# Kernel tuning notes

Hardware: AMD Instinct MI355X
Metric: run time of the kernel (lower is better)

## Reference

```python
import jax, jax.numpy as jnp
import numpy as np

B, T, E = 8, 1024, 512
H = 1024            # hidden_dim
NH, QD, VD = 4, 256, 512
C1, C2 = 512, 2     # conv1_out, conv2_out
K, PAD = 3, 1


def conv1d(x, w, b, pad):
    # x: [B, Cin, T], w: [Cout, Cin, K]
    y = jax.lax.conv_general_dilated(x, w, (1,), [(pad, pad)],
                                     dimension_numbers=('NCH', 'OIH', 'NCH'))
    return y + b[None, :, None]


def setup_inputs() -> dict:
    key = jax.random.key(0)
    ks = jax.random.split(key, 24)
    n = lambda i, shape, s=0.02: jax.random.normal(ks[i], shape, dtype=jnp.float32) * s
    inp = {
        'x':    jax.random.normal(ks[0], (B, T, E), dtype=jnp.float32),
        # in_pro: two 1x1 convs over channels (acting as linears)
        'w_in1': n(1, (E, E)), 'b_in1': jnp.zeros((E,), jnp.float32),
        'w_in2': n(2, (E, E)), 'b_in2': jnp.zeros((E,), jnp.float32),
        # attention projections
        'w_q': n(3, (NH * QD, E), float(np.sqrt(2.0 / (E + QD)))), 'b_q': jnp.zeros((NH * QD,), jnp.float32),
        'w_k': n(4, (NH * QD, E), float(np.sqrt(2.0 / (E + QD)))), 'b_k': jnp.zeros((NH * QD,), jnp.float32),
        'w_v': n(5, (NH * VD, E), float(np.sqrt(2.0 / (E + VD)))), 'b_v': jnp.zeros((NH * VD,), jnp.float32),
        # output projection (1x1 conv)
        'w_p': n(6, (E, NH * VD)), 'b_p': jnp.zeros((E,), jnp.float32),
        # layernorm
        'ln_g': jnp.ones((E,), jnp.float32), 'ln_b': jnp.zeros((E,), jnp.float32),
        # LSTM (1 layer, unidirectional, hidden H)
        'w_ih': n(7, (4 * H, E)), 'w_hh': n(8, (4 * H, H)),
        'b_ih': jnp.zeros((4 * H,), jnp.float32), 'b_hh': jnp.zeros((4 * H,), jnp.float32),
        # attention pooling convs
        'w_c1': n(9, (C1, H, K)), 'b_c1': jnp.zeros((C1,), jnp.float32),
        'w_c2': n(10, (C2, C1, K)), 'b_c2': jnp.zeros((C2,), jnp.float32),
    }
    return inp


def reference(x, w_in1, b_in1, w_in2, b_in2, w_q, b_q, w_k, b_k, w_v, b_v,
              w_p, b_p, ln_g, ln_b, w_ih, w_hh, b_ih, b_hh,
              w_c1, b_c1, w_c2, b_c2):
    # in_pro: 1x1 conv -> LeakyReLU(0.25) -> 1x1 conv (channel-wise linears)
    h = jnp.einsum('bte,fe->btf', x, w_in1) + b_in1
    h = jnp.where(h >= 0, h, 0.25 * h)
    h = jnp.einsum('bte,fe->btf', h, w_in2) + b_in2  # [B,T,E]

    # multi-head attention (no scale factor, as in the source)
    q = (jnp.einsum('bte,fe->btf', h, w_q) + b_q).reshape(B, T, NH, QD)
    k = (jnp.einsum('bte,fe->btf', h, w_k) + b_k).reshape(B, T, NH, QD)
    v = (jnp.einsum('bte,fe->btf', h, w_v) + b_v).reshape(B, T, NH, VD)
    scores = jnp.einsum('btnd,bsnd->bnts', q, k)          # [B,NH,T,T]
    attn = jax.nn.softmax(scores, axis=-1)
    o = jnp.einsum('bnts,bsnd->btnd', attn, v)            # [B,T,NH,VD]
    o = o.reshape(B, T, NH * VD)

    # p_conv1 (1x1) then LayerNorm over E
    y = jnp.einsum('btc,ec->bte', o, w_p) + b_p           # [B,T,E]
    mu = jnp.mean(y, axis=-1, keepdims=True)
    var = jnp.mean(jnp.square(y - mu), axis=-1, keepdims=True)
    y = (y - mu) * jax.lax.rsqrt(var + 1e-5) * ln_g + ln_b

    # LSTM (batch_first, 1 layer); dropout is identity in eval mode
    def step(carry, xt):
        hprev, cprev = carry
        g = xt @ w_ih.T + hprev @ w_hh.T + b_ih + b_hh    # [B,4H]
        i, f, gg, og = jnp.split(g, 4, axis=-1)
        c = jax.nn.sigmoid(f) * cprev + jax.nn.sigmoid(i) * jnp.tanh(gg)
        hn = jax.nn.sigmoid(og) * jnp.tanh(c)
        return (hn, c), hn
    init = (jnp.zeros((B, H), y.dtype), jnp.zeros((B, H), y.dtype))
    _, hs = jax.lax.scan(step, init, jnp.swapaxes(y, 0, 1))  # [T,B,H]
    lstm_out = jnp.swapaxes(hs, 0, 1)                        # [B,T,H]

    # conv-based attention pooling
    a = conv1d(jnp.swapaxes(lstm_out, 1, 2), w_c1, b_c1, PAD)  # [B,C1,T]
    a = jax.nn.relu(a)
    a = conv1d(a, w_c2, b_c2, PAD)                              # [B,C2,T]
    a = jax.nn.softmax(a, axis=2)
    feat = jnp.einsum('bct,bth->bch', a, lstm_out)              # [B,C2,H]
    return feat.reshape(B, C2 * H)
```

## Files before the change

### kernel.cpp

```cpp
#include <hip/hip_runtime.h>
#include <stdint.h>

typedef short short8 __attribute__((ext_vector_type(8)));
typedef float float4v __attribute__((ext_vector_type(4)));

__device__ __forceinline__ float b2f(short s) {
    return __uint_as_float(((unsigned)(unsigned short)s) << 16);
}
__device__ __forceinline__ short f2b(float f) {
    unsigned u = __float_as_uint(f);
    unsigned r = (u + 0x7fffu + ((u >> 16) & 1u)) >> 16;
    return (short)r;
}

__global__ void k_f32_to_bf16(const float* __restrict__ in, short* __restrict__ out, int n) {
    int i = blockIdx.x * blockDim.x + threadIdx.x;
    int stride = gridDim.x * blockDim.x;
    for (; i < n; i += stride) out[i] = f2b(in[i]);
}

__global__ void k_wc1_tr(const float* __restrict__ in, short* __restrict__ out) {
    int i = blockIdx.x * blockDim.x + threadIdx.x;
    if (i >= 512 * 3072) return;
    int c = i / 3072, rr = i % 3072, dk = rr / 1024, h = rr % 1024;
    out[i] = f2b(in[(c * 1024 + h) * 3 + dk]);
}

__global__ void k_bias_sum(const float* __restrict__ a, const float* __restrict__ b,
                           float* __restrict__ o, int n) {
    int i = blockIdx.x * blockDim.x + threadIdx.x;
    if (i < n) o[i] = a[i] + b[i];
}

__global__ __launch_bounds__(256) void k_gemm_bt(
    const short* __restrict__ A, const short* __restrict__ B,
    float* __restrict__ Cf, short* __restrict__ Cb,
    const float* __restrict__ bias,
    int M, int N, int K, int lda, int ldb, int ldc,
    int z0n, long sA0, long sA1, long sB0, long sB1, long sC0, long sC1,
    int act, int gap)
{
    __shared__ __align__(16) short lds[2 * 128 * 32];
    const int z = blockIdx.z;
    const int z0 = z % z0n, z1 = z / z0n;
    A += z1 * sA1 + z0 * sA0;
    B += z1 * sB1 + z0 * sB0;
    const long coff = z1 * sC1 + z0 * sC0;
    const int tn0 = blockIdx.x * 128, tm0 = blockIdx.y * 128;
    const int tid = threadIdx.x, ln = tid & 63, wv = tid >> 6;
    const int wr = wv >> 1, wc = wv & 1;

    float4v acc[4][4];
#pragma unroll
    for (int i = 0; i < 4; ++i)
#pragma unroll
        for (int j = 0; j < 4; ++j) acc[i][j] = (float4v){0.f, 0.f, 0.f, 0.f};

    const int nk = K >> 5;
    for (int kt = 0; kt < nk; ++kt) {
        __syncthreads();
#pragma unroll
        for (int s = 0; s < 4; ++s) {
            int p = tid + (s << 8);
            int pp = p & 511;
            int row = pp >> 2;
            int gcol = (pp & 3) ^ ((pp >> 3) & 3);
            short8 val;
            if (p < 512) {
                long grow = (long)(tm0 + row);
                if (gap) grow += 2 * (grow >> 10);
                val = *(const short8*)&A[grow * (long)lda + kt * 32 + gcol * 8];
            } else {
                val = *(const short8*)&B[(long)(tn0 + row) * ldb + kt * 32 + gcol * 8];
            }
            ((short8*)lds)[(p < 512 ? 0 : 512) + pp] = val;
        }
        __syncthreads();

        short8 af[4], bf_[4];
        const int q = ln >> 4;
#pragma unroll
        for (int i = 0; i < 4; ++i) {
            int r = wr * 64 + i * 16 + (ln & 15);
            af[i] = ((short8*)lds)[r * 4 + (q ^ ((r >> 1) & 3))];
        }
#pragma unroll
        for (int j = 0; j < 4; ++j) {
            int r = wc * 64 + j * 16 + (ln & 15);
            bf_[j] = ((short8*)lds)[512 + r * 4 + (q ^ ((r >> 1) & 3))];
        }
#pragma unroll
        for (int i = 0; i < 4; ++i)
#pragma unroll
            for (int j = 0; j < 4; ++j)
                acc[i][j] = __builtin_amdgcn_mfma_f32_16x16x32_bf16(af[i], bf_[j], acc[i][j], 0, 0, 0);
    }

#pragma unroll
    for (int j = 0; j < 4; ++j) {
        int nglob = tn0 + wc * 64 + j * 16 + (ln & 15);
        float bv = bias ? bias[nglob] : 0.f;
#pragma unroll
        for (int i = 0; i < 4; ++i) {
#pragma unroll
            for (int r = 0; r < 4; ++r) {
                int mglob = tm0 + wr * 64 + i * 16 + (ln >> 4) * 4 + r;
                float v = acc[i][j][r] + bv;
                if (act == 1) v = (v >= 0.f) ? v : 0.25f * v;
                else if (act == 2) v = fmaxf(v, 0.f);
                long ci = coff + (long)mglob * ldc + nglob;
                if (Cf) Cf[ci] = v;
                if (Cb) Cb[ci] = f2b(v);
            }
        }
    }
}

__global__ __launch_bounds__(256) void k_softmax_rows_bf16(short* __restrict__ p) {
    long row = blockIdx.x;
    short* r = p + (row << 10);
    int tid = threadIdx.x;
    float v[4];
    float mx = -3.4e38f;
#pragma unroll
    for (int i = 0; i < 4; ++i) { v[i] = b2f(r[tid + (i << 8)]); mx = fmaxf(mx, v[i]); }
#pragma unroll
    for (int d = 32; d > 0; d >>= 1) mx = fmaxf(mx, __shfl_down(mx, d));
    __shared__ float red[4], red2[4];
    if ((tid & 63) == 0) red[tid >> 6] = mx;
    __syncthreads();
    mx = fmaxf(fmaxf(red[0], red[1]), fmaxf(red[2], red[3]));
    float s = 0.f;
#pragma unroll
    for (int i = 0; i < 4; ++i) { v[i] = expf(v[i] - mx); s += v[i]; }
#pragma unroll
    for (int d = 32; d > 0; d >>= 1) s += __shfl_down(s, d);
    if ((tid & 63) == 0) red2[tid >> 6] = s;
    __syncthreads();
    s = red2[0] + red2[1] + red2[2] + red2[3];
    float inv = 1.f / s;
#pragma unroll
    for (int i = 0; i < 4; ++i) r[tid + (i << 8)] = f2b(v[i] * inv);
}

__global__ __launch_bounds__(256) void k_softmax_rows_f32(float* __restrict__ p) {
    long row = blockIdx.x;
    float* r = p + (row << 10);
    int tid = threadIdx.x;
    float v[4];
    float mx = -3.4e38f;
#pragma unroll
    for (int i = 0; i < 4; ++i) { v[i] = r[tid + (i << 8)]; mx = fmaxf(mx, v[i]); }
#pragma unroll
    for (int d = 32; d > 0; d >>= 1) mx = fmaxf(mx, __shfl_down(mx, d));
    __shared__ float red[4], red2[4];
    if ((tid & 63) == 0) red[tid >> 6] = mx;
    __syncthreads();
    mx = fmaxf(fmaxf(red[0], red[1]), fmaxf(red[2], red[3]));
    float s = 0.f;
#pragma unroll
    for (int i = 0; i < 4; ++i) { v[i] = expf(v[i] - mx); s += v[i]; }
#pragma unroll
    for (int d = 32; d > 0; d >>= 1) s += __shfl_down(s, d);
    if ((tid & 63) == 0) red2[tid >> 6] = s;
    __syncthreads();
    s = red2[0] + red2[1] + red2[2] + red2[3];
    float inv = 1.f / s;
#pragma unroll
    for (int i = 0; i < 4; ++i) r[tid + (i << 8)] = v[i] * inv;
}

__global__ __launch_bounds__(256) void k_layernorm(const short* __restrict__ y,
                                                   const float* __restrict__ gam,
                                                   const float* __restrict__ bet,
                                                   short* __restrict__ o) {
    const long row = blockIdx.x;
    const short* r = y + (row << 9);
    const int tid = threadIdx.x;
    float v0 = b2f(r[tid]), v1 = b2f(r[tid + 256]);
    float s = v0 + v1, ss = v0 * v0 + v1 * v1;
#pragma unroll
    for (int d = 32; d > 0; d >>= 1) { s += __shfl_down(s, d); ss += __shfl_down(ss, d); }
    __shared__ float rs_[4], rss[4];
    if ((tid & 63) == 0) { rs_[tid >> 6] = s; rss[tid >> 6] = ss; }
    __syncthreads();
    s = rs_[0] + rs_[1] + rs_[2] + rs_[3];
    ss = rss[0] + rss[1] + rss[2] + rss[3];
    float mean = s * (1.f / 512.f);
    float var = ss * (1.f / 512.f) - mean * mean;
    float rstd = rsqrtf(var + 1e-5f);
    short* out = o + (row << 9);
    out[tid]       = f2b((v0 - mean) * rstd * gam[tid]       + bet[tid]);
    out[tid + 256] = f2b((v1 - mean) * rstd * gam[tid + 256] + bet[tid + 256]);
}

__global__ __launch_bounds__(256) void k_vT(const short* __restrict__ v, short* __restrict__ vT) {
    __shared__ short t[32][34];
    int bn = blockIdx.z, b = bn >> 2, n = bn & 3;
    int s0 = blockIdx.y * 32, d0 = blockIdx.x * 32;
    int lx = threadIdx.x & 31, ly = threadIdx.x >> 5;
#pragma unroll
    for (int i = 0; i < 4; ++i) {
        int s = ly + i * 8;
        t[s][lx] = v[(long)(b * 1024 + s0 + s) * 2048 + n * 512 + d0 + lx];
    }
    __syncthreads();
#pragma unroll
    for (int i = 0; i < 4; ++i) {
        int d = ly + i * 8;
        vT[((long)bn * 512 + d0 + d) * 1024 + s0 + lx] = t[lx][d];
    }
}

__global__ __launch_bounds__(256) void k_lstm(
    const short* __restrict__ whh, const short* __restrict__ igb,
    short* __restrict__ hA, short* __restrict__ hB,
    short* __restrict__ lstm_pad, int* __restrict__ arr)
{
    const int g = blockIdx.x;
    const int tid = threadIdx.x;
    const int ln = tid & 63, wv = tid >> 6;
    const int kbase = wv * 256 + ((ln >> 4) << 3);

    short8 wf[2][8];
#pragma unroll
    for (int nt = 0; nt < 2; ++nt) {
        int n = nt * 16 + (ln & 15);
        int q = n >> 3, r = n & 7;
        long row = (long)q * 1024 + g * 8 + r;
#pragma unroll
        for (int kk = 0; kk < 8; ++kk)
            wf[nt][kk] = *(const short8*)&whh[row * 1024 + kbase + kk * 32];
    }

    __shared__ float part[4][16][33];
    const int gm = tid >> 3, gu = tid & 7;
    float c_prev = 0.f;
    const short8 zero8 = (short8){0, 0, 0, 0, 0, 0, 0, 0};

    float igv[4];
    if (tid < 64) {
#pragma unroll
        for (int qq = 0; qq < 4; ++qq)
            igv[qq] = b2f(igb[((long)gm * 1024 + 0) * 4096 + qq * 1024 + g * 8 + gu]);
    }

    for (int step = 0; step < 1024; ++step) {
        const short* hp = (step & 1) ? hB : hA;
        short* hn = (step & 1) ? hA : hB;

        short8 af[8];
        {
            const int arow = ln & 15;
            if (arow < 8) {
                const unsigned long long* hq =
                    (const unsigned long long*)(hp + arow * 1024 + kbase);
#pragma unroll
                for (int kk = 0; kk < 8; ++kk) {
                    union { unsigned long long u[2]; short8 s; } cv;
                    cv.u[0] = __hip_atomic_load(hq + kk * 8,     __ATOMIC_RELAXED, __HIP_MEMORY_SCOPE_AGENT);
                    cv.u[1] = __hip_atomic_load(hq + kk * 8 + 1, __ATOMIC_RELAXED, __HIP_MEMORY_SCOPE_AGENT);
                    af[kk] = cv.s;
                }
            } else {
#pragma unroll
                for (int kk = 0; kk < 8; ++kk) af[kk] = zero8;
            }
        }
        float4v acc0 = (float4v){0.f, 0.f, 0.f, 0.f};
        float4v acc1 = (float4v){0.f, 0.f, 0.f, 0.f};
#pragma unroll
        for (int kk = 0; kk < 8; ++kk) {
            acc0 = __builtin_amdgcn_mfma_f32_16x16x32_bf16(af[kk], wf[0][kk], acc0, 0, 0, 0);
            acc1 = __builtin_amdgcn_mfma_f32_16x16x32_bf16(af[kk], wf[1][kk], acc1, 0, 0, 0);
        }
#pragma unroll
        for (int rr = 0; rr < 4; ++rr) {
            part[wv][(ln >> 4) * 4 + rr][ln & 15]        = acc0[rr];
            part[wv][(ln >> 4) * 4 + rr][16 + (ln & 15)] = acc1[rr];
        }
        __syncthreads();

        if (tid < 64) {
            float gates[4];
#pragma unroll
            for (int qq = 0; qq < 4; ++qq) {
                int nn = qq * 8 + gu;
                gates[qq] = part[0][gm][nn] + part[1][gm][nn] + part[2][gm][nn] + part[3][gm][nn]
                          + igv[qq];
            }
            float iv = 1.f / (1.f + expf(-gates[0]));
            float fv = 1.f / (1.f + expf(-gates[1]));
            float gv = tanhf(gates[2]);
            float ov = 1.f / (1.f + expf(-gates[3]));
            float c = fv * c_prev + iv * gv;
            c_prev = c;
            float h = ov * tanhf(c);
            short hb16 = f2b(h);
            __hip_atomic_store(&hn[gm * 1024 + g * 8 + gu], hb16,
                               __ATOMIC_RELAXED, __HIP_MEMORY_SCOPE_AGENT);
            lstm_pad[((long)gm * 1026 + step + 1) * 1024 + g * 8 + gu] = hb16;
        }

        __syncthreads();
        if (tid == 0)
            __hip_atomic_store(&arr[g], step + 1, __ATOMIC_RELAXED, __HIP_MEMORY_SCOPE_AGENT);
        if (tid < 64 && step + 1 < 1024) {
#pragma unroll
            for (int qq = 0; qq < 4; ++qq)
                igv[qq] = b2f(igb[((long)gm * 1024 + step + 1) * 4096 + qq * 1024 + g * 8 + gu]);
        }
        if (wv == 0) {
            const int target = step + 1;
            while (true) {
                int v0 = __hip_atomic_load(&arr[ln],      __ATOMIC_RELAXED, __HIP_MEMORY_SCOPE_AGENT);
                int v1 = __hip_atomic_load(&arr[ln + 64], __ATOMIC_RELAXED, __HIP_MEMORY_SCOPE_AGENT);
                if (__all(v0 >= target && v1 >= target)) break;
                __builtin_amdgcn_s_sleep(1);
            }
        }
        __syncthreads();
    }
}

__global__ __launch_bounds__(256) void k_conv2(const short* __restrict__ a1,
                                               const float* __restrict__ w,
                                               const float* __restrict__ bias,
                                               float* __restrict__ a2) {
    int idx = blockIdx.x * blockDim.x + threadIdx.x;
    if (idx >= 8 * 2 * 1024) return;
    int t = idx & 1023, c = (idx >> 10) & 1, b = idx >> 11;
    float s = bias[c];
    for (int dk = 0; dk < 3; ++dk) {
        int tt = t + dk - 1;
        if (tt < 0 || tt >= 1024) continue;
        const short* arow = a1 + (long)(b * 1024 + tt) * 512;
        const float* wrow = w + c * 1536 + dk;
        for (int j = 0; j < 512; ++j) s += b2f(arow[j]) * wrow[j * 3];
    }
    a2[idx] = s;
}

__global__ __launch_bounds__(256) void k_feat(const float* __restrict__ attw,
                                              const short* __restrict__ lstm_pad,
                                              float* __restrict__ out) {
    int bc = blockIdx.x;
    int b = bc >> 1;
    int tid = threadIdx.x;
    __shared__ float aw[1024];
    for (int i = tid; i < 1024; i += 256) aw[i] = attw[bc * 1024 + i];
    __syncthreads();
    float acc[4] = {0.f, 0.f, 0.f, 0.f};
    for (int t = 0; t < 1024; ++t) {
        float a = aw[t];
        const short* hrow = lstm_pad + ((long)(b * 1026 + t + 1)) * 1024;
#pragma unroll
        for (int i = 0; i < 4; ++i) acc[i] += a * b2f(hrow[tid + (i << 8)]);
    }
#pragma unroll
    for (int i = 0; i < 4; ++i) out[bc * 1024 + tid + (i << 8)] = acc[i];
}

static void gemm_bt(hipStream_t st, const short* A, const short* B, float* Cf, short* Cb,
                    const float* bias, int M, int N, int K, int lda, int ldb, int ldc,
                    int z, int z0n, long sA0, long sA1, long sB0, long sB1, long sC0, long sC1,
                    int act, int gap) {
    dim3 grid(N / 128, M / 128, z);
    k_gemm_bt<<<grid, dim3(256), 0, st>>>(A, B, Cf, Cb, bias, M, N, K, lda, ldb, ldc,
                                          z0n, sA0, sA1, sB0, sB1, sC0, sC1, act, gap);
}

static void cvt(hipStream_t st, const float* in, short* out, int n) {
    int blocks = (n / 4 + 255) / 256;
    if (blocks < 1) blocks = 1;
    k_f32_to_bf16<<<dim3(blocks), dim3(256), 0, st>>>(in, out, n);
}

extern "C" void kernel_launch(void* const* d_in, const int* in_sizes, int n_in,
                              void* d_out, int out_size, void* d_ws, size_t ws_size,
                              hipStream_t stream) {
    if (ws_size < 199409920u) return;

    const float* x     = (const float*)d_in[0];
    const float* w_in1 = (const float*)d_in[1];
    const float* b_in1 = (const float*)d_in[2];
    const float* w_in2 = (const float*)d_in[3];
    const float* b_in2 = (const float*)d_in[4];
    const float* w_q   = (const float*)d_in[5];
    const float* b_q   = (const float*)d_in[6];
    const float* w_k   = (const float*)d_in[7];
    const float* b_k   = (const float*)d_in[8];
    const float* w_v   = (const float*)d_in[9];
    const float* b_v   = (const float*)d_in[10];
    const float* w_p   = (const float*)d_in[11];
    const float* b_p   = (const float*)d_in[12];
    const float* ln_g  = (const float*)d_in[13];
    const float* ln_b  = (const float*)d_in[14];
    const float* w_ih  = (const float*)d_in[15];
    const float* w_hh  = (const float*)d_in[16];
    const float* b_ih  = (const float*)d_in[17];
    const float* b_hh  = (const float*)d_in[18];
    const float* w_c1  = (const float*)d_in[19];
    const float* b_c1  = (const float*)d_in[20];
    const float* w_c2  = (const float*)d_in[21];
    const float* b_c2  = (const float*)d_in[22];

    char* ws = (char*)d_ws;
    short* w1b  = (short*)(ws + 0);
    short* w2b  = (short*)(ws + 524288);
    short* wqb  = (short*)(ws + 1048576);
    short* wkb  = (short*)(ws + 2097152);
    short* wvb  = (short*)(ws + 3145728);
    short* wpb  = (short*)(ws + 5242880);
    short* wihb = (short*)(ws + 7340032);
    short* whhb = (short*)(ws + 11534336);
    short* wc1b = (short*)(ws + 19922944);
    float* bsum = (float*)(ws + 23068672);
    short* hs0  = (short*)(ws + 23085056);
    short* hs1  = (short*)(ws + 23117824);
    int*   arr  = (int*)  (ws + 23150592);
    float* a2   = (float*)(ws + 23150848);
    short* lpad = (short*)(ws + 23216384);
    const size_t D0 = 40026368u;
    short* xbf   = (short*)(ws + D0);
    short* h1bf  = (short*)(ws + D0 + 8388608);
    short* h2bf  = (short*)(ws + D0 + 16777216);
    short* qbf   = (short*)(ws + D0 + 25165824);
    short* kbf   = (short*)(ws + D0 + 41943040);
    short* vbf   = (short*)(ws + D0 + 58720256);
    short* vTbf  = (short*)(ws + D0 + 92274688);
    short* scb   = (short*)(ws + D0);
    short* obf   = (short*)(ws + D0 + 125829120);
    short* ybf   = (short*)(ws + D0 + 58720256);
    short* ylnbf = (short*)(ws + D0 + 67108864);
    short* igb   = (short*)(ws + D0 + 92274688);
    short* a1bf  = (short*)(ws + D0);

    hipMemsetAsync(lpad, 0, (size_t)8 * 1026 * 1024 * 2, stream);
    hipMemsetAsync(hs0, 0, 32768, stream);
    hipMemsetAsync(hs1, 0, 32768, stream);
    hipMemsetAsync(arr, 0, 256, stream);

    cvt(stream, x, xbf, 8192 * 512);
    cvt(stream, w_in1, w1b, 512 * 512);
    cvt(stream, w_in2, w2b, 512 * 512);
    cvt(stream, w_q, wqb, 1024 * 512);
    cvt(stream, w_k, wkb, 1024 * 512);
    cvt(stream, w_v, wvb, 2048 * 512);
    cvt(stream, w_p, wpb, 512 * 2048);
    cvt(stream, w_ih, wihb, 4096 * 512);
    cvt(stream, w_hh, whhb, 4096 * 1024);
    k_wc1_tr<<<dim3((512 * 3072 + 255) / 256), dim3(256), 0, stream>>>(w_c1, wc1b);
    k_bias_sum<<<dim3(16), dim3(256), 0, stream>>>(b_ih, b_hh, bsum, 4096);

    gemm_bt(stream, xbf, w1b, nullptr, h1bf, b_in1, 8192, 512, 512, 512, 512, 512,
            1, 1, 0, 0, 0, 0, 0, 0, 1, 0);
    gemm_bt(stream, h1bf, w2b, nullptr, h2bf, b_in2, 8192, 512, 512, 512, 512, 512,
            1, 1, 0, 0, 0, 0, 0, 0, 0, 0);
    gemm_bt(stream, h2bf, wqb, nullptr, qbf, b_q, 8192, 1024, 512, 512, 512, 1024,
            1, 1, 0, 0, 0, 0, 0, 0, 0, 0);
    gemm_bt(stream, h2bf, wkb, nullptr, kbf, b_k, 8192, 1024, 512, 512, 512, 1024,
            1, 1, 0, 0, 0, 0, 0, 0, 0, 0);
    gemm_bt(stream, h2bf, wvb, nullptr, vbf, b_v, 8192, 2048, 512, 512, 512, 2048,
            1, 1, 0, 0, 0, 0, 0, 0, 0, 0);
    k_vT<<<dim3(16, 32, 32), dim3(256), 0, stream>>>(vbf, vTbf);

    for (int b = 0; b < 8; ++b) {
        const short* qb = qbf + (long)b * 1048576;
        const short* kb = kbf + (long)b * 1048576;
        gemm_bt(stream, qb, kb, nullptr, scb, nullptr, 1024, 1024, 256, 1024, 1024, 1024,
                4, 4, 256, 0, 256, 0, 1048576, 0, 0, 0);
        k_softmax_rows_bf16<<<dim3(4096), dim3(256), 0, stream>>>(scb);
        gemm_bt(stream, scb, vTbf + (long)b * 2097152, nullptr, obf + (long)b * 2097152, nullptr,
                1024, 512, 1024, 1024, 1024, 2048, 4, 4, 1048576, 0, 524288, 0, 512, 0, 0, 0);
    }

    gemm_bt(stream, obf, wpb, nullptr, ybf, b_p, 8192, 512, 2048, 2048, 2048, 512,
            1, 1, 0, 0, 0, 0, 0, 0, 0, 0);
    k_layernorm<<<dim3(8192), dim3(256), 0, stream>>>(ybf, ln_g, ln_b, ylnbf);
    gemm_bt(stream, ylnbf, wihb, nullptr, igb, bsum, 8192, 4096, 512, 512, 512, 4096,
            1, 1, 0, 0, 0, 0, 0, 0, 0, 0);
    k_lstm<<<dim3(128), dim3(256), 0, stream>>>(whhb, igb, hs0, hs1, lpad, arr);
    gemm_bt(stream, lpad, wc1b, nullptr, a1bf, b_c1, 8192, 512, 3072, 1024, 3072, 512,
            1, 1, 0, 0, 0, 0, 0, 0, 2, 1);
    k_conv2<<<dim3(64), dim3(256), 0, stream>>>(a1bf, w_c2, b_c2, a2);
    k_softmax_rows_f32<<<dim3(16), dim3(256), 0, stream>>>(a2);
    k_feat<<<dim3(16), dim3(256), 0, stream>>>(a2, lpad, (float*)d_out);
    (void)in_sizes; (void)n_in; (void)out_size; (void)ws_size;
}
```

Baseline: 4.459 ms.

## Tag hidden-state words with step to replace LSTM grid barrier, batch attention launches

The LSTM kernel drops the per-step arrival-counter grid barrier. Each hidden value is now stored as a 32-bit word packing the bf16 value with its step number, and consumers poll until every tag matches. This removes one global round trip and a block barrier per step, at the cost of 32-bit loads per element and spinning on data words. It also uses fast exp-based sigmoid and tanh, merges the weight conversions into one launch, and processes two batches per attention launch group to halve launch count.

```diff
diff --git a/kernel.cpp b/kernel.cpp
--- a/kernel.cpp
+++ b/kernel.cpp
@@ -17,6 +17,27 @@
     int i = blockIdx.x * blockDim.x + threadIdx.x;
     int stride = gridDim.x * blockDim.x;
     for (; i < n; i += stride) out[i] = f2b(in[i]);
+}
+
+__global__ void k_cvt_weights(const float* __restrict__ s0, const float* __restrict__ s1,
+                              const float* __restrict__ s2, const float* __restrict__ s3,
+                              const float* __restrict__ s4, const float* __restrict__ s5,
+                              const float* __restrict__ s6, const float* __restrict__ s7,
+                              short* __restrict__ dst) {
+    int i = blockIdx.x * blockDim.x + threadIdx.x;
+    int stride = gridDim.x * blockDim.x;
+    for (; i < 9961472; i += stride) {
+        float v;
+        if      (i <  262144) v = s0[i];
+        else if (i <  524288) v = s1[i -  262144];
+        else if (i < 1048576) v = s2[i -  524288];
+        else if (i < 1572864) v = s3[i - 1048576];
+        else if (i < 2621440) v = s4[i - 1572864];
+        else if (i < 3670016) v = s5[i - 2621440];
+        else if (i < 5767168) v = s6[i - 3670016];
+        else                  v = s7[i - 5767168];
+        dst[i] = f2b(v);
+    }
 }
 
 __global__ void k_wc1_tr(const float* __restrict__ in, short* __restrict__ out) {
@@ -214,8 +235,8 @@
 
 __global__ __launch_bounds__(256) void k_lstm(
     const short* __restrict__ whh, const short* __restrict__ igb,
-    short* __restrict__ hA, short* __restrict__ hB,
-    short* __restrict__ lstm_pad, int* __restrict__ arr)
+    unsigned int* __restrict__ ht,
+    short* __restrict__ lstm_pad)
 {
     const int g = blockIdx.x;
     const int tid = threadIdx.x;
@@ -236,7 +257,8 @@
     __shared__ float part[4][16][33];
     const int gm = tid >> 3, gu = tid & 7;
     float c_prev = 0.f;
-    const short8 zero8 = (short8){0, 0, 0, 0, 0, 0, 0, 0};
+    const int arow = ln & 15;
+    const bool act8 = (arow < 8);
 
     float igv[4];
     if (tid < 64) {
@@ -245,28 +267,48 @@
             igv[qq] = b2f(igb[((long)gm * 1024 + 0) * 4096 + qq * 1024 + g * 8 + gu]);
     }
 
+    unsigned int w[8][8];
+
     for (int step = 0; step < 1024; ++step) {
-        const short* hp = (step & 1) ? hB : hA;
-        short* hn = (step & 1) ? hA : hB;
+        const unsigned tag = (unsigned)step;
+        const unsigned int* hw = ht + ((step & 1) << 13) + (arow << 10) + kbase;
+
+        if (act8) {
+#pragma unroll
+            for (int kk = 0; kk < 8; ++kk)
+#pragma unroll
+                for (int j = 0; j < 8; ++j)
+                    w[kk][j] = __hip_atomic_load(hw + kk * 32 + j,
+                                                 __ATOMIC_RELAXED, __HIP_MEMORY_SCOPE_AGENT);
+        }
+        while (true) {
+            unsigned bad = 0;
+            if (act8) {
+#pragma unroll
+                for (int kk = 0; kk < 8; ++kk)
+#pragma unroll
+                    for (int j = 0; j < 8; ++j)
+                        bad |= (w[kk][j] ^ tag) & 0xffffu;
+            }
+            if (__all(bad == 0)) break;
+            __builtin_amdgcn_s_sleep(1);
+            if (act8) {
+#pragma unroll
+                for (int kk = 0; kk < 8; ++kk)
+#pragma unroll
+                    for (int j = 0; j < 8; ++j)
+                        w[kk][j] = __hip_atomic_load(hw + kk * 32 + j,
+                                                     __ATOMIC_RELAXED, __HIP_MEMORY_SCOPE_AGENT);
+            }
+        }
 
         short8 af[8];
-        {
-            const int arow = ln & 15;
-            if (arow < 8) {
-                const unsigned long long* hq =
-                    (const unsigned long long*)(hp + arow * 1024 + kbase);
-#pragma unroll
-                for (int kk = 0; kk < 8; ++kk) {
-                    union { unsigned long long u[2]; short8 s; } cv;
-                    cv.u[0] = __hip_atomic_load(hq + kk * 8,     __ATOMIC_RELAXED, __HIP_MEMORY_SCOPE_AGENT);
-                    cv.u[1] = __hip_atomic_load(hq + kk * 8 + 1, __ATOMIC_RELAXED, __HIP_MEMORY_SCOPE_AGENT);
-                    af[kk] = cv.s;
-                }
-            } else {
-#pragma unroll
-                for (int kk = 0; kk < 8; ++kk) af[kk] = zero8;
-            }
-        }
+#pragma unroll
+        for (int kk = 0; kk < 8; ++kk)
+#pragma unroll
+            for (int j = 0; j < 8; ++j)
+                af[kk][j] = act8 ? (short)(w[kk][j] >> 16) : (short)0;
+
         float4v acc0 = (float4v){0.f, 0.f, 0.f, 0.f};
         float4v acc1 = (float4v){0.f, 0.f, 0.f, 0.f};
 #pragma unroll
@@ -281,45 +323,39 @@
         }
         __syncthreads();
 
+        float psum[4];
         if (tid < 64) {
-            float gates[4];
 #pragma unroll
             for (int qq = 0; qq < 4; ++qq) {
                 int nn = qq * 8 + gu;
-                gates[qq] = part[0][gm][nn] + part[1][gm][nn] + part[2][gm][nn] + part[3][gm][nn]
-                          + igv[qq];
+                psum[qq] = part[0][gm][nn] + part[1][gm][nn] + part[2][gm][nn] + part[3][gm][nn];
             }
-            float iv = 1.f / (1.f + expf(-gates[0]));
-            float fv = 1.f / (1.f + expf(-gates[1]));
-            float gv = tanhf(gates[2]);
-            float ov = 1.f / (1.f + expf(-gates[3]));
+        }
+        __syncthreads();
+
+        if (tid < 64) {
+            float g0 = psum[0] + igv[0];
+            float g1 = psum[1] + igv[1];
+            float g2 = psum[2] + igv[2];
+            float g3 = psum[3] + igv[3];
+            float iv = 1.f / (1.f + __expf(-g0));
+            float fv = 1.f / (1.f + __expf(-g1));
+            float gv = 2.f / (1.f + __expf(-2.f * g2)) - 1.f;
+            float ov = 1.f / (1.f + __expf(-g3));
             float c = fv * c_prev + iv * gv;
             c_prev = c;
-            float h = ov * tanhf(c);
+            float h = ov * (2.f / (1.f + __expf(-2.f * c)) - 1.f);
             short hb16 = f2b(h);
-            __hip_atomic_store(&hn[gm * 1024 + g * 8 + gu], hb16,
-                               __ATOMIC_RELAXED, __HIP_MEMORY_SCOPE_AGENT);
+            unsigned word = ((unsigned)(unsigned short)hb16 << 16) | (unsigned)(step + 1);
+            __hip_atomic_store(ht + (((step + 1) & 1) << 13) + (gm << 10) + g * 8 + gu,
+                               word, __ATOMIC_RELAXED, __HIP_MEMORY_SCOPE_AGENT);
             lstm_pad[((long)gm * 1026 + step + 1) * 1024 + g * 8 + gu] = hb16;
-        }
-
-        __syncthreads();
-        if (tid == 0)
-            __hip_atomic_store(&arr[g], step + 1, __ATOMIC_RELAXED, __HIP_MEMORY_SCOPE_AGENT);
-        if (tid < 64 && step + 1 < 1024) {
-#pragma unroll
-            for (int qq = 0; qq < 4; ++qq)
-                igv[qq] = b2f(igb[((long)gm * 1024 + step + 1) * 4096 + qq * 1024 + g * 8 + gu]);
-        }
-        if (wv == 0) {
-            const int target = step + 1;
-            while (true) {
-                int v0 = __hip_atomic_load(&arr[ln],      __ATOMIC_RELAXED, __HIP_MEMORY_SCOPE_AGENT);
-                int v1 = __hip_atomic_load(&arr[ln + 64], __ATOMIC_RELAXED, __HIP_MEMORY_SCOPE_AGENT);
-                if (__all(v0 >= target && v1 >= target)) break;
-                __builtin_amdgcn_s_sleep(1);
+            if (step + 1 < 1024) {
+#pragma unroll
+                for (int qq = 0; qq < 4; ++qq)
+                    igv[qq] = b2f(igb[((long)gm * 1024 + step + 1) * 4096 + qq * 1024 + g * 8 + gu]);
             }
         }
-        __syncthreads();
     }
 }
 
@@ -368,12 +404,6 @@
     dim3 grid(N / 128, M / 128, z);
     k_gemm_bt<<<grid, dim3(256), 0, st>>>(A, B, Cf, Cb, bias, M, N, K, lda, ldb, ldc,
                                           z0n, sA0, sA1, sB0, sB1, sC0, sC1, act, gap);
-}
-
-static void cvt(hipStream_t st, const float* in, short* out, int n) {
-    int blocks = (n / 4 + 255) / 256;
-    if (blocks < 1) blocks = 1;
-    k_f32_to_bf16<<<dim3(blocks), dim3(256), 0, st>>>(in, out, n);
 }
 
 extern "C" void kernel_launch(void* const* d_in, const int* in_sizes, int n_in,
@@ -407,20 +437,18 @@
 
     char* ws = (char*)d_ws;
     short* w1b  = (short*)(ws + 0);
+    short* wihb = (short*)(ws + 7340032);
+    short* wc1b = (short*)(ws + 19922944);
+    float* bsum = (float*)(ws + 23068672);
+    unsigned int* ht = (unsigned int*)(ws + 23085056);
+    float* a2   = (float*)(ws + 23150848);
+    short* lpad = (short*)(ws + 23216384);
     short* w2b  = (short*)(ws + 524288);
     short* wqb  = (short*)(ws + 1048576);
     short* wkb  = (short*)(ws + 2097152);
     short* wvb  = (short*)(ws + 3145728);
     short* wpb  = (short*)(ws + 5242880);
-    short* wihb = (short*)(ws + 7340032);
     short* whhb = (short*)(ws + 11534336);
-    short* wc1b = (short*)(ws + 19922944);
-    float* bsum = (float*)(ws + 23068672);
-    short* hs0  = (short*)(ws + 23085056);
-    short* hs1  = (short*)(ws + 23117824);
-    int*   arr  = (int*)  (ws + 23150592);
-    float* a2   = (float*)(ws + 23150848);
-    short* lpad = (short*)(ws + 23216384);
     const size_t D0 = 40026368u;
     short* xbf   = (short*)(ws + D0);
     short* h1bf  = (short*)(ws + D0 + 8388608);
@@ -437,19 +465,11 @@
     short* a1bf  = (short*)(ws + D0);
 
     hipMemsetAsync(lpad, 0, (size_t)8 * 1026 * 1024 * 2, stream);
-    hipMemsetAsync(hs0, 0, 32768, stream);
-    hipMemsetAsync(hs1, 0, 32768, stream);
-    hipMemsetAsync(arr, 0, 256, stream);
-
-    cvt(stream, x, xbf, 8192 * 512);
-    cvt(stream, w_in1, w1b, 512 * 512);
-    cvt(stream, w_in2, w2b, 512 * 512);
-    cvt(stream, w_q, wqb, 1024 * 512);
-    cvt(stream, w_k, wkb, 1024 * 512);
-    cvt(stream, w_v, wvb, 2048 * 512);
-    cvt(stream, w_p, wpb, 512 * 2048);
-    cvt(stream, w_ih, wihb, 4096 * 512);
-    cvt(stream, w_hh, whhb, 4096 * 1024);
+    hipMemsetAsync(ht, 0, 65536, stream);
+
+    k_f32_to_bf16<<<dim3(4096), dim3(256), 0, stream>>>(x, xbf, 8192 * 512);
+    k_cvt_weights<<<dim3(4096), dim3(256), 0, stream>>>(w_in1, w_in2, w_q, w_k, w_v, w_p,
+                                                        w_ih, w_hh, w1b);
     k_wc1_tr<<<dim3((512 * 3072 + 255) / 256), dim3(256), 0, stream>>>(w_c1, wc1b);
     k_bias_sum<<<dim3(16), dim3(256), 0, stream>>>(b_ih, b_hh, bsum, 4096);
 
@@ -465,14 +485,15 @@
             1, 1, 0, 0, 0, 0, 0, 0, 0, 0);
     k_vT<<<dim3(16, 32, 32), dim3(256), 0, stream>>>(vbf, vTbf);
 
-    for (int b = 0; b < 8; ++b) {
-        const short* qb = qbf + (long)b * 1048576;
-        const short* kb = kbf + (long)b * 1048576;
+    for (int bg = 0; bg < 4; ++bg) {
+        const short* qb = qbf + (long)bg * 2097152;
+        const short* kb = kbf + (long)bg * 2097152;
         gemm_bt(stream, qb, kb, nullptr, scb, nullptr, 1024, 1024, 256, 1024, 1024, 1024,
-                4, 4, 256, 0, 256, 0, 1048576, 0, 0, 0);
-        k_softmax_rows_bf16<<<dim3(4096), dim3(256), 0, stream>>>(scb);
-        gemm_bt(stream, scb, vTbf + (long)b * 2097152, nullptr, obf + (long)b * 2097152, nullptr,
-                1024, 512, 1024, 1024, 1024, 2048, 4, 4, 1048576, 0, 524288, 0, 512, 0, 0, 0);
+                8, 4, 256, 1048576, 256, 1048576, 1048576, 4194304, 0, 0);
+        k_softmax_rows_bf16<<<dim3(8192), dim3(256), 0, stream>>>(scb);
+        gemm_bt(stream, scb, vTbf + (long)bg * 4194304, nullptr, obf + (long)bg * 4194304, nullptr,
+                1024, 512, 1024, 1024, 1024, 2048,
+                8, 4, 1048576, 4194304, 524288, 2097152, 512, 2097152, 0, 0);
     }
 
     gemm_bt(stream, obf, wpb, nullptr, ybf, b_p, 8192, 512, 2048, 2048, 2048, 512,
@@ -480,7 +501,7 @@
     k_layernorm<<<dim3(8192), dim3(256), 0, stream>>>(ybf, ln_g, ln_b, ylnbf);
     gemm_bt(stream, ylnbf, wihb, nullptr, igb, bsum, 8192, 4096, 512, 512, 512, 4096,
             1, 1, 0, 0, 0, 0, 0, 0, 0, 0);
-    k_lstm<<<dim3(128), dim3(256), 0, stream>>>(whhb, igb, hs0, hs1, lpad, arr);
+    k_lstm<<<dim3(128), dim3(256), 0, stream>>>(whhb, igb, ht, lpad);
     gemm_bt(stream, lpad, wc1b, nullptr, a1bf, b_c1, 8192, 512, 3072, 1024, 3072, 512,
             1, 1, 0, 0, 0, 0, 0, 0, 2, 1);
     k_conv2<<<dim3(64), dim3(256), 0, stream>>>(a1bf, w_c2, b_c2, a2);
```

Result: slower. 11.06 ms (+148.1%).
